# Performance work log

Measured on AMD Instinct MI355X. Metric: run time of the kernel, lower is better.

Reference implementation:

```python
import jax, jax.numpy as jnp
import numpy as np

B, S, D_IN, D_OUT, H = 16, 4096, 1024, 1024, 16
HD = D_OUT // H  # 64
EPS = 1e-6


def setup_inputs() -> dict:
    key = jax.random.key(0)
    ks = jax.random.split(key, 10)
    scale = 1.0 / np.sqrt(D_OUT)
    return {
        "y_superposed": jax.random.normal(ks[0], (B, S, D_OUT), dtype=jnp.float32),
        "x_context": jax.random.normal(ks[1], (B, D_IN), dtype=jnp.float32),
        "Wq": jax.random.normal(ks[2], (D_IN, D_OUT), dtype=jnp.float32) * scale,
        "bq": jnp.zeros((D_OUT,), dtype=jnp.float32),
        "Wk": jax.random.normal(ks[3], (D_OUT, D_OUT), dtype=jnp.float32) * scale,
        "bk": jnp.zeros((D_OUT,), dtype=jnp.float32),
        "Wv": jax.random.normal(ks[4], (D_OUT, D_OUT), dtype=jnp.float32) * scale,
        "bv": jnp.zeros((D_OUT,), dtype=jnp.float32),
        "Wo": jax.random.normal(ks[5], (D_OUT, D_OUT), dtype=jnp.float32) * scale,
        "bo": jnp.zeros((D_OUT,), dtype=jnp.float32),
    }


def _feature_map(x):
    # feature_map_id == 1: elu(x) + 1 (strictly positive kernel feature map)
    return jax.nn.elu(x) + 1.0


def reference(y_superposed, x_context, Wq, bq, Wk, bk, Wv, bv, Wo, bo):
    b = x_context.shape[0]
    # Q from context: [b, d_out] -> [b, H, 1, hd]
    q = (x_context @ Wq + bq).reshape(b, 1, H, HD).transpose(0, 2, 1, 3)
    # K, V from superposed states: [b, S, d_out] -> [b, H, S, hd]
    k = (y_superposed @ Wk + bk).reshape(b, -1, H, HD).transpose(0, 2, 1, 3)
    v = (y_superposed @ Wv + bv).reshape(b, -1, H, HD).transpose(0, 2, 1, 3)
    # Kernel (linear) attention: O(S) path, elu+1 feature map
    phi_q = _feature_map(q)          # [b, H, 1, hd]
    phi_k = _feature_map(k)          # [b, H, S, hd]
    kv = jnp.einsum('bhsd,bhsv->bhdv', phi_k, v)        # [b, H, hd, hd]
    numerator = jnp.einsum('bhqd,bhdv->bhqv', phi_q, kv)  # [b, H, 1, hd]
    k_sum = jnp.sum(phi_k, axis=2, keepdims=True)        # [b, H, 1, hd]
    denominator = jnp.sum(phi_q * k_sum, axis=-1, keepdims=True)  # [b, H, 1, 1]
    ctx = numerator / (denominator + EPS)                # [b, H, 1, hd]
    # Collapse heads back: [b, H, 1, hd] -> [b, d_out]
    ctx = ctx.transpose(0, 2, 1, 3).reshape(b, D_OUT)
    return ctx @ Wo + bo
```

## Files before the change

kernel.cpp:

```cpp
#include <hip/hip_runtime.h>
#include <hip/hip_bf16.h>

#define D   1024
#define S   4096
#define NB  16
#define NH  16
#define NSC 32

using bf16x8 = __attribute__((ext_vector_type(8))) short;
using f32x4  = __attribute__((ext_vector_type(4))) float;

__device__ __forceinline__ short f2bf(float f) {
    unsigned int u = __float_as_uint(f);
    u += 0x7fffu + ((u >> 16) & 1u);
    return (short)(u >> 16);
}
__device__ __forceinline__ unsigned int cvtpk(float a, float b) {
    unsigned int r;
    asm("v_cvt_pk_bf16_f32 %0, %1, %2" : "=v"(r) : "v"(a), "v"(b));
    return r;
}
__device__ __forceinline__ float elu1(float x) {
    return x > 0.f ? x + 1.f : __expf(x);
}

__global__ __launch_bounds__(256) void phiq_kernel(const float* __restrict__ x,
        const float* __restrict__ Wq, const float* __restrict__ bq,
        float* __restrict__ phiq)
{
    const int b = blockIdx.y;
    const int o = blockIdx.x * 256 + threadIdx.x;
    __shared__ float xl[D];
    for (int i = threadIdx.x; i < D; i += 256) xl[i] = x[b * D + i];
    __syncthreads();
    float acc = bq[o];
    for (int j = 0; j < D; ++j) acc = fmaf(xl[j], Wq[(size_t)j * D + o], acc);
    phiq[b * D + o] = elu1(acc);
}

__global__ __launch_bounds__(256) void wkt_kernel(const float* __restrict__ Wk,
        unsigned short* __restrict__ WkT)
{
    __shared__ float tile[32][33];
    const int tx = threadIdx.x & 31, ty = threadIdx.x >> 5;
    const int j0 = blockIdx.y * 32, o0 = blockIdx.x * 32;
#pragma unroll
    for (int r = 0; r < 4; ++r)
        tile[ty + r * 8][tx] = Wk[(size_t)(j0 + ty + r * 8) * D + o0 + tx];
    __syncthreads();
#pragma unroll
    for (int r = 0; r < 4; ++r) {
        const int o = o0 + ty + r * 8;
        WkT[(size_t)o * D + j0 + tx] = (unsigned short)f2bf(tile[tx][ty + r * 8]);
    }
}

__global__ __launch_bounds__(256, 2) void kgemm_kernel(
        const float* __restrict__ y, const unsigned short* __restrict__ WkT,
        const float* __restrict__ phiq, const float* __restrict__ bk,
        float* __restrict__ wbuf)
{
    const int bid = blockIdx.x;
    const int wg  = (bid & 7) * 256 + (bid >> 3);
    const int mt  = wg >> 2;
    const int nt  = wg & 3;
    const int b   = mt >> 5;
    const int s0  = (mt & 31) << 7;
    const int n0  = nt << 8;
    const int t   = threadIdx.x;
    const int wv  = t >> 6;
    const int l   = t & 63;
    const int wr  = wv >> 1, wc = wv & 1;
    const int l15 = l & 15, l16 = l >> 4;

    __shared__ float Af[128 * 64];
    __shared__ short Bl[256 * 64];

    f32x4 acc[4][8] = {};

    const float* yb = y + (size_t)(b * S + s0) * D;

    for (int kt = 0; kt < D / 64; ++kt) {
        const int k0 = kt * 64;
#pragma unroll
        for (int i = 0; i < 8; ++i) {
            const int slot0 = i * 256 + wv * 64;
            const int slot  = slot0 + l;
            const int row   = slot >> 4;
            const int cs    = slot & 15;
            const int ke    = (cs ^ (row & 15)) << 2;
            __builtin_amdgcn_global_load_lds(
                (const __attribute__((address_space(1))) unsigned int*)(yb + (size_t)row * D + k0 + ke),
                (__attribute__((address_space(3))) unsigned int*)(&Af[slot0 * 4]),
                16, 0, 0);
        }
#pragma unroll
        for (int i = 0; i < 8; ++i) {
            const int slot0 = i * 256 + wv * 64;
            const int slot  = slot0 + l;
            const int nrow  = slot >> 3;
            const int ke    = ((slot & 7) ^ (nrow & 7)) << 3;
            __builtin_amdgcn_global_load_lds(
                (const __attribute__((address_space(1))) unsigned int*)(WkT + (size_t)(n0 + nrow) * D + k0 + ke),
                (__attribute__((address_space(3))) unsigned int*)(&Bl[slot0 * 8]),
                16, 0, 0);
        }
        __syncthreads();
#pragma unroll
        for (int kk = 0; kk < 2; ++kk) {
            bf16x8 af[4], bfr[8];
            const int ksA = kk * 8 + l16 * 2;
            const int ksB = (kk << 2) + l16;
#pragma unroll
            for (int m = 0; m < 4; ++m) {
                const int row = wr * 64 + m * 16 + l15;
                const f32x4 lo = *reinterpret_cast<const f32x4*>(
                    &Af[row * 64 + ((ksA ^ (row & 15)) << 2)]);
                const f32x4 hi = *reinterpret_cast<const f32x4*>(
                    &Af[row * 64 + (((ksA + 1) ^ (row & 15)) << 2)]);
                union { unsigned int u[4]; bf16x8 v; } cv;
                cv.u[0] = cvtpk(lo[0], lo[1]);
                cv.u[1] = cvtpk(lo[2], lo[3]);
                cv.u[2] = cvtpk(hi[0], hi[1]);
                cv.u[3] = cvtpk(hi[2], hi[3]);
                af[m] = cv.v;
            }
#pragma unroll
            for (int n = 0; n < 8; ++n) {
                const int row = wc * 128 + n * 16 + l15;
                bfr[n] = *reinterpret_cast<const bf16x8*>(&Bl[row * 64 + ((ksB ^ (row & 7)) << 3)]);
            }
#pragma unroll
            for (int m = 0; m < 4; ++m)
#pragma unroll
                for (int n = 0; n < 8; ++n)
                    acc[m][n] = __builtin_amdgcn_mfma_f32_16x16x32_bf16(af[m], bfr[n], acc[m][n], 0, 0, 0);
        }
        __syncthreads();
    }

    const int h0 = (n0 >> 6) + wc * 2;
    float pq[8], bkv[8];
#pragma unroll
    for (int n = 0; n < 8; ++n) {
        const int col = n0 + wc * 128 + n * 16 + l15;
        pq[n]  = phiq[b * D + col];
        bkv[n] = bk[col];
    }
#pragma unroll
    for (int m = 0; m < 4; ++m) {
#pragma unroll
        for (int j = 0; j < 4; ++j) {
            float rs0 = 0.f, rs1 = 0.f;
#pragma unroll
            for (int n = 0; n < 4; ++n) {
                rs0 += elu1(acc[m][n][j] + bkv[n]) * pq[n];
                rs1 += elu1(acc[m][n + 4][j] + bkv[n + 4]) * pq[n + 4];
            }
            rs0 += __shfl_xor(rs0, 1); rs1 += __shfl_xor(rs1, 1);
            rs0 += __shfl_xor(rs0, 2); rs1 += __shfl_xor(rs1, 2);
            rs0 += __shfl_xor(rs0, 4); rs1 += __shfl_xor(rs1, 4);
            rs0 += __shfl_xor(rs0, 8); rs1 += __shfl_xor(rs1, 8);
            if (l15 == 0) {
                const int row = s0 + wr * 64 + m * 16 + l16 * 4 + j;
                wbuf[(size_t)(b * NH + h0) * S + row]     = rs0;
                wbuf[(size_t)(b * NH + h0 + 1) * S + row] = rs1;
            }
        }
    }
}

__global__ __launch_bounds__(256) void tpart_kernel(
        const float* __restrict__ y, const float* __restrict__ wbuf,
        float* __restrict__ tpart)
{
    const int sc = blockIdx.x;
    const int b  = blockIdx.y;
    const int t  = threadIdx.x;
    const int s0 = sc * 128;
    __shared__ float wl[16 * 128];
#pragma unroll
    for (int r = 0; r < 8; ++r) {
        const int lin = r * 256 + t;
        wl[lin] = wbuf[(size_t)(b * NH + (lin >> 7)) * S + s0 + (lin & 127)];
    }
    __syncthreads();
    float acc[16][4] = {};
    const float* yb = y + (size_t)(b * S + s0) * D + t * 4;
    for (int si = 0; si < 128; ++si) {
        const float4 v = *reinterpret_cast<const float4*>(yb + (size_t)si * D);
#pragma unroll
        for (int hh = 0; hh < 16; ++hh) {
            const float wv = wl[hh * 128 + si];
            acc[hh][0] = fmaf(wv, v.x, acc[hh][0]);
            acc[hh][1] = fmaf(wv, v.y, acc[hh][1]);
            acc[hh][2] = fmaf(wv, v.z, acc[hh][2]);
            acc[hh][3] = fmaf(wv, v.w, acc[hh][3]);
        }
    }
    float* tp = tpart + ((size_t)(sc * NB + b) * NH) * D + t * 4;
#pragma unroll
    for (int hh = 0; hh < 16; ++hh) {
        float4 o;
        o.x = acc[hh][0]; o.y = acc[hh][1]; o.z = acc[hh][2]; o.w = acc[hh][3];
        *reinterpret_cast<float4*>(tp + hh * D) = o;
    }
}

__global__ __launch_bounds__(256) void tred_kernel(const float* __restrict__ tpart,
        float* __restrict__ tbuf)
{
    const int idx = blockIdx.x * 256 + threadIdx.x;
    float s = 0.f;
#pragma unroll
    for (int sc = 0; sc < NSC; ++sc) s += tpart[(size_t)sc * (NB * NH * D) + idx];
    tbuf[idx] = s;
}

__global__ __launch_bounds__(256) void ctx_kernel(
        const float* __restrict__ wbuf, const float* __restrict__ tbuf,
        const float* __restrict__ Wv, const float* __restrict__ bv,
        float* __restrict__ ctx)
{
    const int b = blockIdx.x >> 4, h = blockIdx.x & 15;
    const int t = threadIdx.x;
    const int v = t & 63, jq = t >> 6;
    __shared__ float rnum[256];
    __shared__ float rden[4];
    const float* wr_ = wbuf + (size_t)(b * NH + h) * S;
    float dp = 0.f;
    for (int i = t; i < S; i += 256) dp += wr_[i];
#pragma unroll
    for (int off = 1; off < 64; off <<= 1) dp += __shfl_xor(dp, off);
    if ((t & 63) == 0) rden[t >> 6] = dp;
    const float* tr = tbuf + (size_t)(b * NH + h) * D;
    float np = 0.f;
    for (int j = jq * 256; j < jq * 256 + 256; ++j)
        np = fmaf(tr[j], Wv[(size_t)j * D + h * 64 + v], np);
    rnum[t] = np;
    __syncthreads();
    if (t < 64) {
        const float denom = rden[0] + rden[1] + rden[2] + rden[3];
        float num = rnum[v] + rnum[64 + v] + rnum[128 + v] + rnum[192 + v];
        num += denom * bv[h * 64 + v];
        ctx[(size_t)b * D + h * 64 + v] = num / (denom + 1e-6f);
    }
}

__global__ __launch_bounds__(256) void out_kernel(
        const float* __restrict__ ctx, const float* __restrict__ Wo,
        const float* __restrict__ bo, float* __restrict__ out)
{
    const int b = blockIdx.y;
    const int o = blockIdx.x * 256 + threadIdx.x;
    __shared__ float cl[D];
    for (int i = threadIdx.x; i < D; i += 256) cl[i] = ctx[(size_t)b * D + i];
    __syncthreads();
    float acc = bo[o];
    for (int j = 0; j < D; ++j) acc = fmaf(cl[j], Wo[(size_t)j * D + o], acc);
    out[(size_t)b * D + o] = acc;
}

extern "C" void kernel_launch(void* const* d_in, const int* in_sizes, int n_in,
                              void* d_out, int out_size, void* d_ws, size_t ws_size,
                              hipStream_t stream) {
    const float* y  = (const float*)d_in[0];
    const float* x  = (const float*)d_in[1];
    const float* Wq = (const float*)d_in[2];
    const float* bq = (const float*)d_in[3];
    const float* Wk = (const float*)d_in[4];
    const float* bk = (const float*)d_in[5];
    const float* Wv = (const float*)d_in[6];
    const float* bv = (const float*)d_in[7];
    const float* Wo = (const float*)d_in[8];
    const float* bo = (const float*)d_in[9];
    float* out = (float*)d_out;

    char* ws = (char*)d_ws;
    size_t off = 0;
    unsigned short* WkT  = (unsigned short*)(ws + off); off += (size_t)D * D * 2;
    float*          phiq = (float*)(ws + off);          off += (size_t)NB * D * 4;
    float*          wbuf = (float*)(ws + off);          off += (size_t)NB * NH * S * 4;
    float*          tpart= (float*)(ws + off);          off += (size_t)NSC * NB * NH * D * 4;
    float*          tbuf = (float*)(ws + off);          off += (size_t)NB * NH * D * 4;
    float*          ctx  = (float*)(ws + off);          off += (size_t)NB * D * 4;

    phiq_kernel<<<dim3(4, NB), 256, 0, stream>>>(x, Wq, bq, phiq);
    wkt_kernel <<<dim3(32, 32), 256, 0, stream>>>(Wk, WkT);
    kgemm_kernel<<<2048, 256, 0, stream>>>(y, WkT, phiq, bk, wbuf);
    tpart_kernel<<<dim3(NSC, NB), 256, 0, stream>>>(y, wbuf, tpart);
    tred_kernel <<<1024, 256, 0, stream>>>(tpart, tbuf);
    ctx_kernel  <<<256, 256, 0, stream>>>(wbuf, tbuf, Wv, bv, ctx);
    out_kernel  <<<dim3(4, NB), 256, 0, stream>>>(ctx, Wo, bo, out);
}
```

Before: 325.7 us.

## Use 8 waves per block in K-GEMM with 2x4 wave tiling

The K-projection GEMM block grows from 256 to 512 threads, and the 128x256 output tile is split over a 2x4 wave grid. Each wave now covers a 64x64 sub-tile, which is exactly one head, so the epilogue reduces a single head per wave instead of two. This halves accumulator registers per wave and doubles the waves resident per CU, aiming to hide latency better. In exchange the A fragments are converted from fp32 to bf16 redundantly across more waves, and LDS traffic per MFMA rises.

Measured after the change: 426.1 us. +30.8%, slower.

```diff
diff --git a/kernel.cpp b/kernel.cpp
--- a/kernel.cpp
+++ b/kernel.cpp
@@ -55,7 +55,7 @@
     }
 }
 
-__global__ __launch_bounds__(256, 2) void kgemm_kernel(
+__global__ __launch_bounds__(512, 2) void kgemm_kernel(
         const float* __restrict__ y, const unsigned short* __restrict__ WkT,
         const float* __restrict__ phiq, const float* __restrict__ bk,
         float* __restrict__ wbuf)
@@ -70,21 +70,21 @@
     const int t   = threadIdx.x;
     const int wv  = t >> 6;
     const int l   = t & 63;
-    const int wr  = wv >> 1, wc = wv & 1;
+    const int wm  = wv >> 2, wn = wv & 3;
     const int l15 = l & 15, l16 = l >> 4;
 
     __shared__ float Af[128 * 64];
     __shared__ short Bl[256 * 64];
 
-    f32x4 acc[4][8] = {};
+    f32x4 acc[4][4] = {};
 
     const float* yb = y + (size_t)(b * S + s0) * D;
 
     for (int kt = 0; kt < D / 64; ++kt) {
         const int k0 = kt * 64;
 #pragma unroll
-        for (int i = 0; i < 8; ++i) {
-            const int slot0 = i * 256 + wv * 64;
+        for (int i = 0; i < 4; ++i) {
+            const int slot0 = i * 512 + wv * 64;
             const int slot  = slot0 + l;
             const int row   = slot >> 4;
             const int cs    = slot & 15;
@@ -95,8 +95,8 @@
                 16, 0, 0);
         }
 #pragma unroll
-        for (int i = 0; i < 8; ++i) {
-            const int slot0 = i * 256 + wv * 64;
+        for (int i = 0; i < 4; ++i) {
+            const int slot0 = i * 512 + wv * 64;
             const int slot  = slot0 + l;
             const int nrow  = slot >> 3;
             const int ke    = ((slot & 7) ^ (nrow & 7)) << 3;
@@ -108,12 +108,12 @@
         __syncthreads();
 #pragma unroll
         for (int kk = 0; kk < 2; ++kk) {
-            bf16x8 af[4], bfr[8];
+            bf16x8 af[4], bfr[4];
             const int ksA = kk * 8 + l16 * 2;
             const int ksB = (kk << 2) + l16;
 #pragma unroll
             for (int m = 0; m < 4; ++m) {
-                const int row = wr * 64 + m * 16 + l15;
+                const int row = wm * 64 + m * 16 + l15;
                 const f32x4 lo = *reinterpret_cast<const f32x4*>(
                     &Af[row * 64 + ((ksA ^ (row & 15)) << 2)]);
                 const f32x4 hi = *reinterpret_cast<const f32x4*>(
@@ -126,24 +126,24 @@
                 af[m] = cv.v;
             }
 #pragma unroll
-            for (int n = 0; n < 8; ++n) {
-                const int row = wc * 128 + n * 16 + l15;
+            for (int n = 0; n < 4; ++n) {
+                const int row = wn * 64 + n * 16 + l15;
                 bfr[n] = *reinterpret_cast<const bf16x8*>(&Bl[row * 64 + ((ksB ^ (row & 7)) << 3)]);
             }
 #pragma unroll
             for (int m = 0; m < 4; ++m)
 #pragma unroll
-                for (int n = 0; n < 8; ++n)
+                for (int n = 0; n < 4; ++n)
                     acc[m][n] = __builtin_amdgcn_mfma_f32_16x16x32_bf16(af[m], bfr[n], acc[m][n], 0, 0, 0);
         }
         __syncthreads();
     }
 
-    const int h0 = (n0 >> 6) + wc * 2;
-    float pq[8], bkv[8];
-#pragma unroll
-    for (int n = 0; n < 8; ++n) {
-        const int col = n0 + wc * 128 + n * 16 + l15;
+    const int h = nt * 4 + wn;
+    float pq[4], bkv[4];
+#pragma unroll
+    for (int n = 0; n < 4; ++n) {
+        const int col = n0 + wn * 64 + n * 16 + l15;
         pq[n]  = phiq[b * D + col];
         bkv[n] = bk[col];
     }
@@ -151,20 +151,17 @@
     for (int m = 0; m < 4; ++m) {
 #pragma unroll
         for (int j = 0; j < 4; ++j) {
-            float rs0 = 0.f, rs1 = 0.f;
-#pragma unroll
-            for (int n = 0; n < 4; ++n) {
-                rs0 += elu1(acc[m][n][j] + bkv[n]) * pq[n];
-                rs1 += elu1(acc[m][n + 4][j] + bkv[n + 4]) * pq[n + 4];
-            }
-            rs0 += __shfl_xor(rs0, 1); rs1 += __shfl_xor(rs1, 1);
-            rs0 += __shfl_xor(rs0, 2); rs1 += __shfl_xor(rs1, 2);
-            rs0 += __shfl_xor(rs0, 4); rs1 += __shfl_xor(rs1, 4);
-            rs0 += __shfl_xor(rs0, 8); rs1 += __shfl_xor(rs1, 8);
+            float rs = 0.f;
+#pragma unroll
+            for (int n = 0; n < 4; ++n)
+                rs += elu1(acc[m][n][j] + bkv[n]) * pq[n];
+            rs += __shfl_xor(rs, 1);
+            rs += __shfl_xor(rs, 2);
+            rs += __shfl_xor(rs, 4);
+            rs += __shfl_xor(rs, 8);
             if (l15 == 0) {
-                const int row = s0 + wr * 64 + m * 16 + l16 * 4 + j;
-                wbuf[(size_t)(b * NH + h0) * S + row]     = rs0;
-                wbuf[(size_t)(b * NH + h0 + 1) * S + row] = rs1;
+                const int row = s0 + wm * 64 + m * 16 + l16 * 4 + j;
+                wbuf[(size_t)(b * NH + h) * S + row] = rs;
             }
         }
     }
@@ -287,7 +284,7 @@
 
     phiq_kernel<<<dim3(4, NB), 256, 0, stream>>>(x, Wq, bq, phiq);
     wkt_kernel <<<dim3(32, 32), 256, 0, stream>>>(Wk, WkT);
-    kgemm_kernel<<<2048, 256, 0, stream>>>(y, WkT, phiq, bk, wbuf);
+    kgemm_kernel<<<2048, 512, 0, stream>>>(y, WkT, phiq, bk, wbuf);
     tpart_kernel<<<dim3(NSC, NB), 256, 0, stream>>>(y, wbuf, tpart);
     tred_kernel <<<1024, 256, 0, stream>>>(tpart, tbuf);
     ctx_kernel  <<<256, 256, 0, stream>>>(wbuf, tbuf, Wv, bv, ctx);
```
